# Performance work log

Measured on AMD Instinct MI355X. Metric: run time of the kernel, lower is better.

The kernel has to match this reference:

```python
import jax, jax.numpy as jnp
import numpy as np

NEG_SLOPE = 0.2  # DGL GATConv default leaky_relu slope
N_LIG, E_LIG = 10000, 80000
N_REC, E_REC = 30000, 480000
B = 32  # graphs per batch


def setup_inputs() -> dict:
    key = jax.random.key(0)
    ks = jax.random.split(key, 32)
    d = {}
    d["x_lig"] = jax.random.normal(ks[0], (N_LIG, 64), jnp.float32)
    d["src_lig"] = jax.random.randint(ks[1], (E_LIG,), 0, N_LIG, jnp.int32)
    d["dst_lig"] = jax.random.randint(ks[2], (E_LIG,), 0, N_LIG, jnp.int32)
    d["gid_lig"] = jnp.sort(jax.random.randint(ks[3], (N_LIG,), 0, B, jnp.int32))
    d["x_rec"] = jax.random.normal(ks[4], (N_REC, 64), jnp.float32)
    d["src_rec"] = jax.random.randint(ks[5], (E_REC,), 0, N_REC, jnp.int32)
    d["dst_rec"] = jax.random.randint(ks[6], (E_REC,), 0, N_REC, jnp.int32)
    d["gid_rec"] = jnp.sort(jax.random.randint(ks[7], (N_REC,), 0, B, jnp.int32))
    s = 0.1
    # GAT layer 1 (lig): 64 -> 10 heads x 64 ; layer 2: 64 -> 1 head x 128
    d["W1l"] = s * jax.random.normal(ks[8], (64, 10 * 64), jnp.float32)
    d["al1l"] = s * jax.random.normal(ks[9], (10, 64), jnp.float32)
    d["ar1l"] = s * jax.random.normal(ks[10], (10, 64), jnp.float32)
    d["b1l"] = jnp.zeros((10, 64), jnp.float32)
    d["W2l"] = s * jax.random.normal(ks[11], (64, 128), jnp.float32)
    d["al2l"] = s * jax.random.normal(ks[12], (1, 128), jnp.float32)
    d["ar2l"] = s * jax.random.normal(ks[13], (1, 128), jnp.float32)
    d["b2l"] = jnp.zeros((1, 128), jnp.float32)
    d["W1r"] = s * jax.random.normal(ks[14], (64, 10 * 64), jnp.float32)
    d["al1r"] = s * jax.random.normal(ks[15], (10, 64), jnp.float32)
    d["ar1r"] = s * jax.random.normal(ks[16], (10, 64), jnp.float32)
    d["b1r"] = jnp.zeros((10, 64), jnp.float32)
    d["W2r"] = s * jax.random.normal(ks[17], (64, 128), jnp.float32)
    d["al2r"] = s * jax.random.normal(ks[18], (1, 128), jnp.float32)
    d["ar2r"] = s * jax.random.normal(ks[19], (1, 128), jnp.float32)
    d["b2r"] = jnp.zeros((1, 128), jnp.float32)
    d["W_lin1"] = s * jax.random.normal(ks[20], (256, 128), jnp.float32)
    d["b_lin1"] = jnp.zeros((128,), jnp.float32)
    d["W_lin2"] = s * jax.random.normal(ks[21], (128, 1), jnp.float32)
    d["b_lin2"] = jnp.zeros((1,), jnp.float32)
    return d


def gat_conv(x, src, dst, W, al, ar, b, num_nodes):
    # DGL GATConv (eval mode: dropouts off). al/ar: [H, D]
    H, D = al.shape
    h = (x @ W).reshape(num_nodes, H, D)          # [N, H, D]
    el = jnp.einsum("nhd,hd->nh", h, al)          # [N, H]
    er = jnp.einsum("nhd,hd->nh", h, ar)
    e = jax.nn.leaky_relu(el[src] + er[dst], NEG_SLOPE)   # [E, H]
    # edge softmax over incoming edges of each dst node
    emax = jax.ops.segment_max(e, dst, num_segments=num_nodes)
    ex = jnp.exp(e - emax[dst])
    denom = jax.ops.segment_sum(ex, dst, num_segments=num_nodes)
    alpha = ex / denom[dst]                       # [E, H]
    msg = alpha[:, :, None] * h[src]              # [E, H, D]
    out = jax.ops.segment_sum(msg, dst, num_segments=num_nodes)
    return out + b[None]                          # [N, H, D]


def branch(x, src, dst, gid, W1, al1, ar1, b1, W2, al2, ar2, b2):
    n = x.shape[0]
    h = jax.nn.relu(gat_conv(x, src, dst, W1, al1, ar1, b1, n)).sum(axis=1)  # sum heads -> [N, 64]
    h = jax.nn.relu(gat_conv(h, src, dst, W2, al2, ar2, b2, n))[:, 0, :]     # [N, 128]
    return jax.ops.segment_max(h, gid, num_segments=B)                       # max readout [B, 128]


def reference(x_lig, src_lig, dst_lig, gid_lig, x_rec, src_rec, dst_rec, gid_rec,
              W1l, al1l, ar1l, b1l, W2l, al2l, ar2l, b2l,
              W1r, al1r, ar1r, b1r, W2r, al2r, ar2r, b2r,
              W_lin1, b_lin1, W_lin2, b_lin2):
    hlig = branch(x_lig, src_lig, dst_lig, gid_lig, W1l, al1l, ar1l, b1l, W2l, al2l, ar2l, b2l)
    hrec = branch(x_rec, src_rec, dst_rec, gid_rec, W1r, al1r, ar1r, b1r, W2r, al2r, ar2r, b2r)
    h = jnp.concatenate([hlig, hrec], axis=-1)    # [B, 256]
    h = jax.nn.relu(h @ W_lin1 + b_lin1)
    h = jax.nn.relu(h @ W_lin2 + b_lin2)
    return h.flatten()                            # [B]
```

## Files before the change

### kernel.cpp

```cpp
#include <hip/hip_runtime.h>

#define LRELU(x) fmaxf((x), 0.2f*(x))
#define ZPAD(f) ((f) + 4*((f)>>6))

static inline int cdiv(int a, int b) { return (a + b - 1) / b; }

template<int H, int DH>
__global__ void prep_wal2_kernel(const float* __restrict__ WA, const float* __restrict__ alA,
                                 const float* __restrict__ arA, float* __restrict__ walA,
                                 float* __restrict__ warA, int nbA,
                                 const float* __restrict__ WB, const float* __restrict__ alB,
                                 const float* __restrict__ arB, float* __restrict__ walB,
                                 float* __restrict__ warB) {
  constexpr int K = 64;
  constexpr int HD = H * DH;
  const float *W, *al, *ar; float *wal, *war; int bid;
  if (blockIdx.x < (unsigned)nbA) { W=WA; al=alA; ar=arA; wal=walA; war=warA; bid=blockIdx.x; }
  else { W=WB; al=alB; ar=arB; wal=walB; war=warB; bid=blockIdx.x-nbA; }
  const int wv = threadIdx.x >> 6, lane = threadIdx.x & 63;
  const int o = bid * (blockDim.x >> 6) + wv;
  if (o >= H * K) return;
  const int h = o / K, k = o - h * K;
  float pl = 0.f, pr = 0.f;
#pragma unroll
  for (int j = 0; j < DH / 64; j++) {
    int d = j * 64 + lane;
    float w = W[(size_t)k * HD + h * DH + d];
    pl += w * al[h * DH + d];
    pr += w * ar[h * DH + d];
  }
#pragma unroll
  for (int off = 32; off >= 1; off >>= 1) {
    pl += __shfl_xor(pl, off);
    pr += __shfl_xor(pr, off);
  }
  if (lane == 0) { wal[o] = pl; war[o] = pr; }
}

__global__ void elr10_2_kernel(const float* __restrict__ xA, const float* __restrict__ walA,
                               const float* __restrict__ warA, float* __restrict__ elA,
                               float* __restrict__ erA, int NA, int nbA,
                               const float* __restrict__ xB, const float* __restrict__ walB,
                               const float* __restrict__ warB, float* __restrict__ elB,
                               float* __restrict__ erB, int NB) {
  const float *x, *wal, *war; float *el, *er; int N, bid;
  if (blockIdx.x < (unsigned)nbA) { x=xA; wal=walA; war=warA; el=elA; er=erA; N=NA; bid=blockIdx.x; }
  else { x=xB; wal=walB; war=warB; el=elB; er=erB; N=NB; bid=blockIdx.x-nbA; }
  const int wv = threadIdx.x >> 6, lane = threadIdx.x & 63;
  const int n = bid * (blockDim.x >> 6) + wv;
  if (n >= N) return;
  const float xv = x[(size_t)n * 64 + lane];
#pragma unroll
  for (int h = 0; h < 10; h++) {
    float pl = xv * wal[h * 64 + lane];
    float pr = xv * war[h * 64 + lane];
#pragma unroll
    for (int off = 32; off >= 1; off >>= 1) {
      pl += __shfl_xor(pl, off);
      pr += __shfl_xor(pr, off);
    }
    if (lane == 0) { el[(size_t)n * 10 + h] = pl; er[(size_t)n * 10 + h] = pr; }
  }
}

__global__ void deg2_kernel(const int* __restrict__ dstA, int* __restrict__ degA, int EA, int nbA,
                            const int* __restrict__ dstB, int* __restrict__ degB, int EB) {
  const int* dst; int* deg; int E, t;
  if (blockIdx.x < (unsigned)nbA) { dst=dstA; deg=degA; E=EA; t=blockIdx.x*256+threadIdx.x; }
  else { dst=dstB; deg=degB; E=EB; t=(blockIdx.x-nbA)*256+threadIdx.x; }
  if (t < E) atomicAdd(&deg[dst[t]], 1);
}

__global__ void rowptr2_kernel(const int* __restrict__ degA, int* __restrict__ rpA,
                               int* __restrict__ curA, int* __restrict__ cntA, int NA, int nbA,
                               const int* __restrict__ degB, int* __restrict__ rpB,
                               int* __restrict__ curB, int* __restrict__ cntB, int NB) {
  const int* deg; int *rp, *cur, *cnt; int N, t;
  if (blockIdx.x < (unsigned)nbA) { deg=degA; rp=rpA; cur=curA; cnt=cntA; N=NA; t=blockIdx.x*256+threadIdx.x; }
  else { deg=degB; rp=rpB; cur=curB; cnt=cntB; N=NB; t=(blockIdx.x-nbA)*256+threadIdx.x; }
  int lane = threadIdx.x & 63;
  int v = (t < N) ? deg[t] : 0;
  int x = v;
#pragma unroll
  for (int off = 1; off < 64; off <<= 1) {
    int y = __shfl_up(x, off);
    if (lane >= off) x += y;
  }
  int total = __shfl(x, 63);
  int base = 0;
  if (lane == 0 && total > 0) base = atomicAdd(cnt, total);
  base = __shfl(base, 0);
  int excl = base + x - v;
  if (t < N) { rp[t] = excl; cur[t] = excl; }
}

__global__ void scatter2_kernel(const int* __restrict__ srcA, const int* __restrict__ dstA,
                                int* __restrict__ curA, int* __restrict__ outA, int EA, int nbA,
                                const int* __restrict__ srcB, const int* __restrict__ dstB,
                                int* __restrict__ curB, int* __restrict__ outB, int EB) {
  const int *src, *dst; int *cur, *out; int E, t;
  if (blockIdx.x < (unsigned)nbA) { src=srcA; dst=dstA; cur=curA; out=outA; E=EA; t=blockIdx.x*256+threadIdx.x; }
  else { src=srcB; dst=dstB; cur=curB; out=outB; E=EB; t=(blockIdx.x-nbA)*256+threadIdx.x; }
  if (t >= E) return;
  int slot = atomicAdd(&cur[dst[t]], 1);
  out[slot] = src[t];
}

__global__ void aggr_z10_2_kernel(const int* __restrict__ rpA, const int* __restrict__ degA,
                                  const int* __restrict__ srcsA, const float* __restrict__ xA,
                                  const float* __restrict__ elA, const float* __restrict__ erA,
                                  float* __restrict__ zA, int NA, int nbA,
                                  const int* __restrict__ rpB, const int* __restrict__ degB,
                                  const int* __restrict__ srcsB, const float* __restrict__ xB,
                                  const float* __restrict__ elB, const float* __restrict__ erB,
                                  float* __restrict__ zB, int NB) {
  const int *rp, *degp, *srcs; const float *x, *el, *er; float *z; int N, bid;
  if (blockIdx.x < (unsigned)nbA) { rp=rpA; degp=degA; srcs=srcsA; x=xA; el=elA; er=erA; z=zA; N=NA; bid=blockIdx.x; }
  else { rp=rpB; degp=degB; srcs=srcsB; x=xB; el=elB; er=erB; z=zB; N=NB; bid=blockIdx.x-nbA; }
  const int wv = threadIdx.x >> 6, lane = threadIdx.x & 63;
  const int n = bid * (blockDim.x >> 6) + wv;
  if (n >= N) return;
  const int beg = rp[n], dg = degp[n];
  const float2* elv = (const float2*)el;
  const float2* erv = (const float2*)er;
  float ern[10];
#pragma unroll
  for (int j = 0; j < 5; j++) {
    float2 t2 = erv[(size_t)n * 5 + j];
    ern[2 * j] = t2.x; ern[2 * j + 1] = t2.y;
  }
  float den[10], acc[10];
#pragma unroll
  for (int h = 0; h < 10; h++) { den[h] = 0.f; acc[h] = 0.f; }
  int i = 0;
  for (; i + 1 < dg; i += 2) {
    int s0 = srcs[beg + i], s1 = srcs[beg + i + 1];
    float xv0 = x[(size_t)s0 * 64 + lane];
    float xv1 = x[(size_t)s1 * 64 + lane];
    float w0[10], w1[10];
#pragma unroll
    for (int j = 0; j < 5; j++) {
      float2 a = elv[(size_t)s0 * 5 + j];
      float2 c = elv[(size_t)s1 * 5 + j];
      w0[2 * j] = a.x; w0[2 * j + 1] = a.y;
      w1[2 * j] = c.x; w1[2 * j + 1] = c.y;
    }
#pragma unroll
    for (int h = 0; h < 10; h++) {
      float ea = __expf(LRELU(w0[h] + ern[h]));
      float eb = __expf(LRELU(w1[h] + ern[h]));
      den[h] += ea + eb;
      acc[h] += ea * xv0 + eb * xv1;
    }
  }
  if (i < dg) {
    int s0 = srcs[beg + i];
    float xv0 = x[(size_t)s0 * 64 + lane];
    float w0[10];
#pragma unroll
    for (int j = 0; j < 5; j++) {
      float2 a = elv[(size_t)s0 * 5 + j];
      w0[2 * j] = a.x; w0[2 * j + 1] = a.y;
    }
#pragma unroll
    for (int h = 0; h < 10; h++) {
      float ea = __expf(LRELU(w0[h] + ern[h]));
      den[h] += ea;
      acc[h] += ea * xv0;
    }
  }
#pragma unroll
  for (int h = 0; h < 10; h++)
    z[(size_t)n * 640 + h * 64 + lane] = (dg > 0) ? acc[h] / den[h] : 0.f;
}

__global__ void aggr_z1_2_kernel(const int* __restrict__ rpA, const int* __restrict__ degA,
                                 const int* __restrict__ srcsA, const float* __restrict__ hA,
                                 const float* __restrict__ elA, const float* __restrict__ erA,
                                 float* __restrict__ zA, int NA, int nbA,
                                 const int* __restrict__ rpB, const int* __restrict__ degB,
                                 const int* __restrict__ srcsB, const float* __restrict__ hB,
                                 const float* __restrict__ elB, const float* __restrict__ erB,
                                 float* __restrict__ zB, int NB) {
  const int *rp, *degp, *srcs; const float *hin, *el, *er; float *z; int N, bid;
  if (blockIdx.x < (unsigned)nbA) { rp=rpA; degp=degA; srcs=srcsA; hin=hA; el=elA; er=erA; z=zA; N=NA; bid=blockIdx.x; }
  else { rp=rpB; degp=degB; srcs=srcsB; hin=hB; el=elB; er=erB; z=zB; N=NB; bid=blockIdx.x-nbA; }
  const int wv = threadIdx.x >> 6, lane = threadIdx.x & 63;
  const int n = bid * (blockDim.x >> 6) + wv;
  if (n >= N) return;
  const int beg = rp[n], dg = degp[n];
  const float ern = er[n];
  float den = 0.f, acc = 0.f;
  int i = 0;
  for (; i + 1 < dg; i += 2) {
    int s0 = srcs[beg + i], s1 = srcs[beg + i + 1];
    float x0 = __expf(LRELU(el[s0] + ern));
    float x1 = __expf(LRELU(el[s1] + ern));
    den += x0 + x1;
    acc += x0 * hin[(size_t)s0 * 64 + lane] + x1 * hin[(size_t)s1 * 64 + lane];
  }
  if (i < dg) {
    int s0 = srcs[beg + i];
    float x0 = __expf(LRELU(el[s0] + ern));
    den += x0;
    acc += x0 * hin[(size_t)s0 * 64 + lane];
  }
  z[(size_t)n * 64 + lane] = (dg > 0) ? acc / den : 0.f;
}

__global__ void gemm_sumheads2_kernel(
    const float* __restrict__ zA, const float* __restrict__ WA, const float* __restrict__ bA,
    const float* __restrict__ wal2A, const float* __restrict__ war2A, float* __restrict__ h1A,
    float* __restrict__ el2A, float* __restrict__ er2A, int NA, int nbA,
    const float* __restrict__ zB, const float* __restrict__ WB, const float* __restrict__ bB,
    const float* __restrict__ wal2B, const float* __restrict__ war2B, float* __restrict__ h1B,
    float* __restrict__ el2B, float* __restrict__ er2B, int NB) {
  constexpr int NPB = 16;
  __shared__ float zs[NPB][680];
  const float *z, *W, *bb, *wal2, *war2; float *h1sum, *el2, *er2; int N, tile;
  if (blockIdx.x < (unsigned)nbA) { z=zA; W=WA; bb=bA; wal2=wal2A; war2=war2A; h1sum=h1A; el2=el2A; er2=er2A; N=NA; tile=blockIdx.x; }
  else { z=zB; W=WB; bb=bB; wal2=wal2B; war2=war2B; h1sum=h1B; el2=el2B; er2=er2B; N=NB; tile=blockIdx.x-nbA; }
  const int f = threadIdx.x;
  const int n0 = tile * NPB;
  const int pf = ZPAD(f);
#pragma unroll
  for (int i = 0; i < NPB; i++) {
    int n = n0 + i;
    zs[i][pf] = (n < N) ? z[(size_t)n * 640 + f] : 0.f;
  }
  __syncthreads();
  const int f4 = f % 160;
  const int ng = f / 160;
  const int head = f4 >> 4;
  const int base = 68 * head;
  float acc[4][4];
#pragma unroll
  for (int i = 0; i < 4; i++)
#pragma unroll
    for (int j = 0; j < 4; j++) acc[i][j] = 0.f;
  const float4* W4 = (const float4*)W;
#pragma unroll 4
  for (int k4 = 0; k4 < 16; k4++) {
    float4 zq[4];
#pragma unroll
    for (int i = 0; i < 4; i++)
      zq[i] = *(const float4*)&zs[ng * 4 + i][base + 4 * k4];
#pragma unroll
    for (int j4 = 0; j4 < 4; j4++) {
      const int k = 4 * k4 + j4;
      const float4 w4 = W4[(size_t)k * 160 + f4];
#pragma unroll
      for (int i = 0; i < 4; i++) {
        const float zv = j4 == 0 ? zq[i].x : j4 == 1 ? zq[i].y : j4 == 2 ? zq[i].z : zq[i].w;
        acc[i][0] = fmaf(zv, w4.x, acc[i][0]);
        acc[i][1] = fmaf(zv, w4.y, acc[i][1]);
        acc[i][2] = fmaf(zv, w4.z, acc[i][2]);
        acc[i][3] = fmaf(zv, w4.w, acc[i][3]);
      }
    }
  }
  const float4 b4 = ((const float4*)bb)[f4];
  __syncthreads();
#pragma unroll
  for (int i = 0; i < 4; i++) {
    float* row = &zs[ng * 4 + i][ZPAD(4 * f4)];
    row[0] = fmaxf(acc[i][0] + b4.x, 0.f);
    row[1] = fmaxf(acc[i][1] + b4.y, 0.f);
    row[2] = fmaxf(acc[i][2] + b4.z, 0.f);
    row[3] = fmaxf(acc[i][3] + b4.w, 0.f);
  }
  __syncthreads();
  const int lane = threadIdx.x & 63;
  for (int idx = threadIdx.x; idx < NPB * 64; idx += 640) {
    const int i = idx >> 6, d = idx & 63;
    float s = 0.f;
#pragma unroll
    for (int h = 0; h < 10; h++) s += zs[i][68 * h + d];
    const int n = n0 + i;
    float pl = s * wal2[d], pr = s * war2[d];
#pragma unroll
    for (int off = 32; off >= 1; off >>= 1) {
      pl += __shfl_xor(pl, off);
      pr += __shfl_xor(pr, off);
    }
    if (n < N) {
      h1sum[(size_t)n * 64 + d] = s;
      if (lane == 0) { el2[n] = pl; er2[n] = pr; }
    }
  }
}

__global__ void gemm2_readout3_kernel(
    const float* __restrict__ zA, const float* __restrict__ WA, const float* __restrict__ bA,
    const int* __restrict__ gidA, int NA, int coA, int nbA,
    const float* __restrict__ zB, const float* __restrict__ WB, const float* __restrict__ bB,
    const int* __restrict__ gidB, int NB, int coB,
    float* __restrict__ readout) {
  constexpr int NPB = 16;
  __shared__ float zs[NPB][64];
  __shared__ float vals[NPB][128];
  __shared__ int gids[NPB];
  const float *z, *W, *bb; const int* gid; int N, colOff, tile;
  if (blockIdx.x < (unsigned)nbA) { z=zA; W=WA; bb=bA; gid=gidA; N=NA; colOff=coA; tile=blockIdx.x; }
  else { z=zB; W=WB; bb=bB; gid=gidB; N=NB; colOff=coB; tile=blockIdx.x-nbA; }
  const int f = threadIdx.x;
  const int n0 = tile * NPB;
  for (int idx = f; idx < NPB * 64; idx += 128) {
    int i = idx >> 6, k = idx & 63;
    int n = n0 + i;
    zs[i][k] = (n < N) ? z[(size_t)n * 64 + k] : 0.f;
  }
  if (f < NPB) gids[f] = (n0 + f < N) ? gid[n0 + f] : -1;
  __syncthreads();
  float acc[NPB];
#pragma unroll
  for (int i = 0; i < NPB; i++) acc[i] = 0.f;
#pragma unroll 4
  for (int k4 = 0; k4 < 16; k4++) {
    const float w0 = W[(size_t)(4 * k4 + 0) * 128 + f];
    const float w1 = W[(size_t)(4 * k4 + 1) * 128 + f];
    const float w2 = W[(size_t)(4 * k4 + 2) * 128 + f];
    const float w3 = W[(size_t)(4 * k4 + 3) * 128 + f];
#pragma unroll
    for (int i = 0; i < NPB; i++) {
      float4 zq = *(const float4*)&zs[i][4 * k4];
      acc[i] = fmaf(zq.x, w0, fmaf(zq.y, w1, fmaf(zq.z, w2, fmaf(zq.w, w3, acc[i]))));
    }
  }
  const float bbf = bb[f];
#pragma unroll
  for (int i = 0; i < NPB; i++) vals[i][f] = fmaxf(acc[i] + bbf, 0.f);
  __syncthreads();
  float run = 0.f;
  int curg = -1;
#pragma unroll
  for (int i = 0; i < NPB; i++) {
    int g = gids[i];
    if (g < 0) break;
    if (g != curg) {
      if (curg >= 0)
        atomicMax((unsigned int*)&readout[curg * 256 + colOff + f], __float_as_uint(run));
      curg = g;
      run = 0.f;
    }
    run = fmaxf(run, vals[i][f]);
  }
  if (curg >= 0)
    atomicMax((unsigned int*)&readout[curg * 256 + colOff + f], __float_as_uint(run));
}

__global__ void mlp_kernel(const float* __restrict__ readout, const float* __restrict__ W1,
                           const float* __restrict__ b1, const float* __restrict__ W2,
                           const float* __restrict__ b2, float* __restrict__ out) {
  int b = blockIdx.x;
  int j = threadIdx.x;
  __shared__ float rs[256];
  rs[j] = readout[b * 256 + j];
  rs[j + 128] = readout[b * 256 + 128 + j];
  __syncthreads();
  float acc = b1[j];
#pragma unroll 8
  for (int k = 0; k < 256; k++) acc += rs[k] * W1[k * 128 + j];
  acc = fmaxf(acc, 0.f);
  float p = acc * W2[j];
#pragma unroll
  for (int off = 32; off >= 1; off >>= 1) p += __shfl_xor(p, off);
  __shared__ float wsum[2];
  if ((threadIdx.x & 63) == 0) wsum[threadIdx.x >> 6] = p;
  __syncthreads();
  if (threadIdx.x == 0) {
    float s = wsum[0] + wsum[1] + b2[0];
    out[b] = fmaxf(s, 0.f);
  }
}

extern "C" void kernel_launch(void* const* d_in, const int* in_sizes, int n_in,
                              void* d_out, int out_size, void* d_ws, size_t ws_size,
                              hipStream_t stream) {
  const float* x_lig = (const float*)d_in[0];
  const int* src_lig = (const int*)d_in[1];
  const int* dst_lig = (const int*)d_in[2];
  const int* gid_lig = (const int*)d_in[3];
  const float* x_rec = (const float*)d_in[4];
  const int* src_rec = (const int*)d_in[5];
  const int* dst_rec = (const int*)d_in[6];
  const int* gid_rec = (const int*)d_in[7];
  const float* W1l = (const float*)d_in[8];
  const float* al1l = (const float*)d_in[9];
  const float* ar1l = (const float*)d_in[10];
  const float* b1l = (const float*)d_in[11];
  const float* W2l = (const float*)d_in[12];
  const float* al2l = (const float*)d_in[13];
  const float* ar2l = (const float*)d_in[14];
  const float* b2l = (const float*)d_in[15];
  const float* W1r = (const float*)d_in[16];
  const float* al1r = (const float*)d_in[17];
  const float* ar1r = (const float*)d_in[18];
  const float* b1r = (const float*)d_in[19];
  const float* W2r = (const float*)d_in[20];
  const float* al2r = (const float*)d_in[21];
  const float* ar2r = (const float*)d_in[22];
  const float* b2r = (const float*)d_in[23];
  const float* W_lin1 = (const float*)d_in[24];
  const float* b_lin1 = (const float*)d_in[25];
  const float* W_lin2 = (const float*)d_in[26];
  const float* b_lin2 = (const float*)d_in[27];

  const int NL = 10000, EL = 80000, NR = 30000, ER = 480000;
  float* p = (float*)d_ws;
  float* zL = p;      p += (size_t)NL * 640;
  float* zR = p;      p += (size_t)NR * 640;
  float* z2L = p;     p += (size_t)NL * 64;
  float* z2R = p;     p += (size_t)NR * 64;
  float* h1L = p;     p += (size_t)NL * 64;
  float* h1R = p;     p += (size_t)NR * 64;
  float* el1L = p;    p += (size_t)NL * 10;
  float* er1L = p;    p += (size_t)NL * 10;
  float* el1R = p;    p += (size_t)NR * 10;
  float* er1R = p;    p += (size_t)NR * 10;
  float* el2L = p;    p += NL;
  float* er2L = p;    p += NL;
  float* el2R = p;    p += NR;
  float* er2R = p;    p += NR;
  float* wal1l = p;   p += 640;
  float* war1l = p;   p += 640;
  float* wal1r = p;   p += 640;
  float* war1r = p;   p += 640;
  float* wal2l = p;   p += 64;
  float* war2l = p;   p += 64;
  float* wal2r = p;   p += 64;
  float* war2r = p;   p += 64;
  float* zero_base = p;
  float* readout = p; p += 32 * 256;
  int* ip = (int*)p;
  int* degL = ip;     ip += NL;
  int* cntL = ip;     ip += 1;
  int* degR = ip;     ip += NR;
  int* cntR = ip;     ip += 1;
  size_t zero_bytes = (size_t)((char*)ip - (char*)zero_base);
  int* rpL = ip;      ip += NL;
  int* curL = ip;     ip += NL;
  int* srcsL = ip;    ip += EL;
  int* rpR = ip;      ip += NR;
  int* curR = ip;     ip += NR;
  int* srcsR = ip;    ip += ER;

  hipMemsetAsync(zero_base, 0, zero_bytes, stream);

  prep_wal2_kernel<10, 64><<<160, 512, 0, stream>>>(W1l, al1l, ar1l, wal1l, war1l, 80,
                                                    W1r, al1r, ar1r, wal1r, war1r);
  prep_wal2_kernel<1, 128><<<16, 512, 0, stream>>>(W2l, al2l, ar2l, wal2l, war2l, 8,
                                                   W2r, al2r, ar2r, wal2r, war2r);
  deg2_kernel<<<cdiv(EL, 256) + cdiv(ER, 256), 256, 0, stream>>>(
      dst_lig, degL, EL, cdiv(EL, 256), dst_rec, degR, ER);
  rowptr2_kernel<<<cdiv(NL, 256) + cdiv(NR, 256), 256, 0, stream>>>(
      degL, rpL, curL, cntL, NL, cdiv(NL, 256), degR, rpR, curR, cntR, NR);
  scatter2_kernel<<<cdiv(EL, 256) + cdiv(ER, 256), 256, 0, stream>>>(
      src_lig, dst_lig, curL, srcsL, EL, cdiv(EL, 256), src_rec, dst_rec, curR, srcsR, ER);
  elr10_2_kernel<<<cdiv(NL, 4) + cdiv(NR, 4), 256, 0, stream>>>(
      x_lig, wal1l, war1l, el1L, er1L, NL, cdiv(NL, 4),
      x_rec, wal1r, war1r, el1R, er1R, NR);
  aggr_z10_2_kernel<<<cdiv(NL, 8) + cdiv(NR, 8), 512, 0, stream>>>(
      rpL, degL, srcsL, x_lig, el1L, er1L, zL, NL, cdiv(NL, 8),
      rpR, degR, srcsR, x_rec, el1R, er1R, zR, NR);
  gemm_sumheads2_kernel<<<cdiv(NL, 16) + cdiv(NR, 16), 640, 0, stream>>>(
      zL, W1l, b1l, wal2l, war2l, h1L, el2L, er2L, NL, cdiv(NL, 16),
      zR, W1r, b1r, wal2r, war2r, h1R, el2R, er2R, NR);
  aggr_z1_2_kernel<<<cdiv(NL, 8) + cdiv(NR, 8), 512, 0, stream>>>(
      rpL, degL, srcsL, h1L, el2L, er2L, z2L, NL, cdiv(NL, 8),
      rpR, degR, srcsR, h1R, el2R, er2R, z2R, NR);
  gemm2_readout3_kernel<<<cdiv(NL, 16) + cdiv(NR, 16), 128, 0, stream>>>(
      z2L, W2l, b2l, gid_lig, NL, 0, cdiv(NL, 16),
      z2R, W2r, b2r, gid_rec, NR, 128, readout);

  mlp_kernel<<<32, 128, 0, stream>>>(readout, W_lin1, b_lin1, W_lin2, b_lin2, (float*)d_out);
}
```

Measured before the change: 503.7 us.

## Precompute per-edge attention exponentials in scatter kernel, store in CSR order

```diff
diff --git a/kernel.cpp b/kernel.cpp
--- a/kernel.cpp
+++ b/kernel.cpp
@@ -94,41 +94,49 @@
   if (t < N) { rp[t] = excl; cur[t] = excl; }
 }
 
-__global__ void scatter2_kernel(const int* __restrict__ srcA, const int* __restrict__ dstA,
-                                int* __restrict__ curA, int* __restrict__ outA, int EA, int nbA,
-                                const int* __restrict__ srcB, const int* __restrict__ dstB,
-                                int* __restrict__ curB, int* __restrict__ outB, int EB) {
-  const int *src, *dst; int *cur, *out; int E, t;
-  if (blockIdx.x < (unsigned)nbA) { src=srcA; dst=dstA; cur=curA; out=outA; E=EA; t=blockIdx.x*256+threadIdx.x; }
-  else { src=srcB; dst=dstB; cur=curB; out=outB; E=EB; t=(blockIdx.x-nbA)*256+threadIdx.x; }
+__global__ void scatter_ex2_kernel(
+    const int* __restrict__ srcA, const int* __restrict__ dstA, int* __restrict__ curA,
+    int* __restrict__ outA, const float* __restrict__ elA, const float* __restrict__ erA,
+    float* __restrict__ exA, int EA, int nbA,
+    const int* __restrict__ srcB, const int* __restrict__ dstB, int* __restrict__ curB,
+    int* __restrict__ outB, const float* __restrict__ elB, const float* __restrict__ erB,
+    float* __restrict__ exB, int EB) {
+  const int *src, *dst; int *cur, *out; const float *el, *er; float *ex; int E, t;
+  if (blockIdx.x < (unsigned)nbA) { src=srcA; dst=dstA; cur=curA; out=outA; el=elA; er=erA; ex=exA; E=EA; t=blockIdx.x*256+threadIdx.x; }
+  else { src=srcB; dst=dstB; cur=curB; out=outB; el=elB; er=erB; ex=exB; E=EB; t=(blockIdx.x-nbA)*256+threadIdx.x; }
   if (t >= E) return;
-  int slot = atomicAdd(&cur[dst[t]], 1);
-  out[slot] = src[t];
+  const int s = src[t], d = dst[t];
+  const int slot = atomicAdd(&cur[d], 1);
+  out[slot] = s;
+  const float2* elv = (const float2*)el;
+  const float2* erv = (const float2*)er;
+  float2* exv = (float2*)ex;
+#pragma unroll
+  for (int j = 0; j < 5; j++) {
+    float2 a = elv[(size_t)s * 5 + j];
+    float2 b = erv[(size_t)d * 5 + j];
+    float2 e;
+    e.x = __expf(LRELU(a.x + b.x));
+    e.y = __expf(LRELU(a.y + b.y));
+    exv[(size_t)slot * 5 + j] = e;
+  }
 }
 
 __global__ void aggr_z10_2_kernel(const int* __restrict__ rpA, const int* __restrict__ degA,
                                   const int* __restrict__ srcsA, const float* __restrict__ xA,
-                                  const float* __restrict__ elA, const float* __restrict__ erA,
-                                  float* __restrict__ zA, int NA, int nbA,
+                                  const float* __restrict__ exA, float* __restrict__ zA,
+                                  int NA, int nbA,
                                   const int* __restrict__ rpB, const int* __restrict__ degB,
                                   const int* __restrict__ srcsB, const float* __restrict__ xB,
-                                  const float* __restrict__ elB, const float* __restrict__ erB,
-                                  float* __restrict__ zB, int NB) {
-  const int *rp, *degp, *srcs; const float *x, *el, *er; float *z; int N, bid;
-  if (blockIdx.x < (unsigned)nbA) { rp=rpA; degp=degA; srcs=srcsA; x=xA; el=elA; er=erA; z=zA; N=NA; bid=blockIdx.x; }
-  else { rp=rpB; degp=degB; srcs=srcsB; x=xB; el=elB; er=erB; z=zB; N=NB; bid=blockIdx.x-nbA; }
+                                  const float* __restrict__ exB, float* __restrict__ zB, int NB) {
+  const int *rp, *degp, *srcs; const float *x, *ex; float *z; int N, bid;
+  if (blockIdx.x < (unsigned)nbA) { rp=rpA; degp=degA; srcs=srcsA; x=xA; ex=exA; z=zA; N=NA; bid=blockIdx.x; }
+  else { rp=rpB; degp=degB; srcs=srcsB; x=xB; ex=exB; z=zB; N=NB; bid=blockIdx.x-nbA; }
   const int wv = threadIdx.x >> 6, lane = threadIdx.x & 63;
   const int n = bid * (blockDim.x >> 6) + wv;
   if (n >= N) return;
   const int beg = rp[n], dg = degp[n];
-  const float2* elv = (const float2*)el;
-  const float2* erv = (const float2*)er;
-  float ern[10];
-#pragma unroll
-  for (int j = 0; j < 5; j++) {
-    float2 t2 = erv[(size_t)n * 5 + j];
-    ern[2 * j] = t2.x; ern[2 * j + 1] = t2.y;
-  }
+  const float2* exv = (const float2*)ex;
   float den[10], acc[10];
 #pragma unroll
   for (int h = 0; h < 10; h++) { den[h] = 0.f; acc[h] = 0.f; }
@@ -137,36 +145,30 @@
     int s0 = srcs[beg + i], s1 = srcs[beg + i + 1];
     float xv0 = x[(size_t)s0 * 64 + lane];
     float xv1 = x[(size_t)s1 * 64 + lane];
-    float w0[10], w1[10];
+    float e0[10], e1[10];
 #pragma unroll
     for (int j = 0; j < 5; j++) {
-      float2 a = elv[(size_t)s0 * 5 + j];
-      float2 c = elv[(size_t)s1 * 5 + j];
-      w0[2 * j] = a.x; w0[2 * j + 1] = a.y;
-      w1[2 * j] = c.x; w1[2 * j + 1] = c.y;
+      float2 a = exv[(size_t)(beg + i) * 5 + j];
+      float2 c = exv[(size_t)(beg + i + 1) * 5 + j];
+      e0[2 * j] = a.x; e0[2 * j + 1] = a.y;
+      e1[2 * j] = c.x; e1[2 * j + 1] = c.y;
     }
 #pragma unroll
     for (int h = 0; h < 10; h++) {
-      float ea = __expf(LRELU(w0[h] + ern[h]));
-      float eb = __expf(LRELU(w1[h] + ern[h]));
-      den[h] += ea + eb;
-      acc[h] += ea * xv0 + eb * xv1;
+      den[h] += e0[h] + e1[h];
+      acc[h] = fmaf(e0[h], xv0, fmaf(e1[h], xv1, acc[h]));
     }
   }
   if (i < dg) {
     int s0 = srcs[beg + i];
     float xv0 = x[(size_t)s0 * 64 + lane];
-    float w0[10];
 #pragma unroll
     for (int j = 0; j < 5; j++) {
-      float2 a = elv[(size_t)s0 * 5 + j];
-      w0[2 * j] = a.x; w0[2 * j + 1] = a.y;
-    }
-#pragma unroll
-    for (int h = 0; h < 10; h++) {
-      float ea = __expf(LRELU(w0[h] + ern[h]));
-      den[h] += ea;
-      acc[h] += ea * xv0;
+      float2 a = exv[(size_t)(beg + i) * 5 + j];
+      den[2 * j] += a.x;
+      den[2 * j + 1] += a.y;
+      acc[2 * j] = fmaf(a.x, xv0, acc[2 * j]);
+      acc[2 * j + 1] = fmaf(a.y, xv0, acc[2 * j + 1]);
     }
   }
 #pragma unroll
@@ -410,6 +412,8 @@
   float* p = (float*)d_ws;
   float* zL = p;      p += (size_t)NL * 640;
   float* zR = p;      p += (size_t)NR * 640;
+  float* ex1L = p;    p += (size_t)EL * 10;
+  float* ex1R = p;    p += (size_t)ER * 10;
   float* z2L = p;     p += (size_t)NL * 64;
   float* z2R = p;     p += (size_t)NR * 64;
   float* h1L = p;     p += (size_t)NL * 64;
@@ -455,14 +459,15 @@
       dst_lig, degL, EL, cdiv(EL, 256), dst_rec, degR, ER);
   rowptr2_kernel<<<cdiv(NL, 256) + cdiv(NR, 256), 256, 0, stream>>>(
       degL, rpL, curL, cntL, NL, cdiv(NL, 256), degR, rpR, curR, cntR, NR);
-  scatter2_kernel<<<cdiv(EL, 256) + cdiv(ER, 256), 256, 0, stream>>>(
-      src_lig, dst_lig, curL, srcsL, EL, cdiv(EL, 256), src_rec, dst_rec, curR, srcsR, ER);
   elr10_2_kernel<<<cdiv(NL, 4) + cdiv(NR, 4), 256, 0, stream>>>(
       x_lig, wal1l, war1l, el1L, er1L, NL, cdiv(NL, 4),
       x_rec, wal1r, war1r, el1R, er1R, NR);
+  scatter_ex2_kernel<<<cdiv(EL, 256) + cdiv(ER, 256), 256, 0, stream>>>(
+      src_lig, dst_lig, curL, srcsL, el1L, er1L, ex1L, EL, cdiv(EL, 256),
+      src_rec, dst_rec, curR, srcsR, el1R, er1R, ex1R, ER);
   aggr_z10_2_kernel<<<cdiv(NL, 8) + cdiv(NR, 8), 512, 0, stream>>>(
-      rpL, degL, srcsL, x_lig, el1L, er1L, zL, NL, cdiv(NL, 8),
-      rpR, degR, srcsR, x_rec, el1R, er1R, zR, NR);
+      rpL, degL, srcsL, x_lig, ex1L, zL, NL, cdiv(NL, 8),
+      rpR, degR, srcsR, x_rec, ex1R, zR, NR);
   gemm_sumheads2_kernel<<<cdiv(NL, 16) + cdiv(NR, 16), 640, 0, stream>>>(
       zL, W1l, b1l, wal2l, war2l, h1L, el2L, er2L, NL, cdiv(NL, 16),
       zR, W1r, b1r, wal2r, war2r, h1R, el2R, er2R, NR);
```

Result: no change. 494.6 us (-1.8%).
